# Kernel optimization log

Measured on AMD Instinct MI355X. Metric: run time of the kernel, lower is better.

Reference implementation:

```python
import jax, jax.numpy as jnp
import numpy as np

# ---- PGA G(3,0,1) tables (metric: e0^2=0, e1^2=e2^2=e3^2=1) ----
METRIC = np.array([0.0, 1.0, 1.0, 1.0])
BLADES = [(), (0,), (1,), (2,), (3,), (0, 1), (0, 2), (0, 3), (1, 2), (1, 3),
          (2, 3), (0, 1, 2), (0, 1, 3), (0, 2, 3), (1, 2, 3), (0, 1, 2, 3)]
IDX = {b: i for i, b in enumerate(BLADES)}


def _sort_sign(lst):
    lst = list(lst)
    sign = 1
    for i in range(len(lst)):
        for j in range(len(lst) - 1 - i):
            if lst[j] > lst[j + 1]:
                lst[j], lst[j + 1] = lst[j + 1], lst[j]
                sign = -sign
    return lst, sign


def _gp(a, b):
    lst, sign = _sort_sign(list(a) + list(b))
    coef = float(sign)
    out, i = [], 0
    while i < len(lst):
        if i + 1 < len(lst) and lst[i] == lst[i + 1]:
            coef *= METRIC[lst[i]]
            i += 2
        else:
            out.append(lst[i])
            i += 1
    return tuple(out), coef


def _outer(a, b):
    if set(a) & set(b):
        return (), 0.0
    lst, sign = _sort_sign(list(a) + list(b))
    return tuple(lst), float(sign)


def _build_tables():
    G = np.zeros((16, 16, 16))
    O = np.zeros((16, 16, 16))
    for i, a in enumerate(BLADES):
        for j, b in enumerate(BLADES):
            bl, c = _gp(a, b)
            if c != 0.0:
                G[IDX[bl], i, j] = c
            bl, c = _outer(a, b)
            if c != 0.0:
                O[IDX[bl], i, j] = c
    # right complement dual: a ^ dual(a) = e0123
    D = np.zeros((16, 16))
    for i, a in enumerate(BLADES):
        comp = tuple(sorted(set(range(4)) - set(a)))
        _, s = _outer(a, comp)
        D[IDX[comp], i] = s
    Dinv = np.linalg.inv(D)
    # join(x, y) = undual(dual(x) ^ dual(y))
    J = np.einsum('km,mpq,pi,qj->kij', Dinv, O, D, D)
    # 9 Pin(3,0,1)-equivariant linear basis maps:
    # 5 grade projections + 4 maps (e0 wedge grade-k part without e0)
    B = np.zeros((9, 16, 16))
    grades = [len(b) for b in BLADES]
    for w in range(5):
        for i, g in enumerate(grades):
            if g == w:
                B[w, i, i] = 1.0
    for w in range(4):
        for i, a in enumerate(BLADES):
            if len(a) == w and 0 not in a:
                bl, c = _outer((0,), a)
                B[5 + w, IDX[bl], i] = c
    return jnp.asarray(G), jnp.asarray(J), jnp.asarray(B)


GP_TBL, JOIN_TBL, EQUI_BASIS = _build_tables()


def equi_linear(x, W):
    # x: [..., c, 16], W: [o, c, 9] -> [..., o, 16]
    M = jnp.einsum('ocw,wab->oacb', W, EQUI_BASIS)  # small: [o,16,c,16]
    return jnp.einsum('oacb,...cb->...oa', M, x)


def setup_inputs() -> dict:
    key = jax.random.key(0)
    k1, k2, k3, k4 = jax.random.split(key, 4)
    B, S, C = 8, 8192, 32
    x = jax.random.normal(k1, (B, S, C, 16), dtype=jnp.float32)
    ref_mv = jax.random.normal(k2, (B, S, 1, 16), dtype=jnp.float32)
    W_bil = jax.random.normal(k3, (2 * 32, C, 9), dtype=jnp.float32) / np.sqrt(9 * C)
    W_out = jax.random.normal(k4, (C, 32, 9), dtype=jnp.float32) / np.sqrt(9 * 32)
    return {"x": x, "ref_mv": ref_mv, "W_bil": W_bil, "W_out": W_out}


def reference(x, ref_mv, W_bil, W_out):
    # project hidden channels -> 2*intermediate = 64 channels
    h = equi_linear(x, W_bil)                      # [B,S,64,16]
    lg, rg, lj, rj = jnp.split(h, 4, axis=-2)      # each [B,S,16,16]
    gp = jnp.einsum('kij,...ci,...cj->...ck', GP_TBL, lg, rg)
    jn = ref_mv[..., 14:15] * jnp.einsum('kij,...ci,...cj->...ck', JOIN_TBL, lj, rj)
    y = jnp.concatenate([gp, jn], axis=-2)         # [B,S,32,16]
    return equi_linear(y, W_out)                   # [B,S,32,16]
```

## Files before the change

kernel.cpp:

```cpp
#include <hip/hip_runtime.h>

typedef float v2f __attribute__((ext_vector_type(2)));

namespace pga {
constexpr int MASKA[16] = {0,1,2,4,8,3,5,9,6,10,12,7,11,13,14,15};
constexpr int IMASK[16] = {0,1,2,5,3,6,8,11,4,7,9,12,10,13,14,15};
constexpr int GR[16]    = {0,1,1,1,1,2,2,2,2,2,2,3,3,3,3,4};

constexpr int osign(int a, int b){
  int c = 0;
  for (int j = 0; j < 4; ++j) if ((b>>j)&1)
    for (int i = j+1; i < 4; ++i) if ((a>>i)&1) ++c;
  return (c&1) ? -1 : 1;
}

struct Tab {
  float gpc[16][16]; int gpk[16][16];
  float jnc[16][16]; int jnk[16][16];
};

constexpr Tab build(){
  Tab t{};
  for (int i = 0; i < 16; ++i) for (int j = 0; j < 16; ++j) {
    const int ma = MASKA[i], mb = MASKA[j];
    if (ma & mb & 1) { t.gpc[i][j] = 0.0f; t.gpk[i][j] = 0; }
    else { t.gpk[i][j] = IMASK[ma^mb]; t.gpc[i][j] = (float)osign(ma, mb); }
    const int ua = 15^ma, ub = 15^mb;
    if (ua & ub) { t.jnc[i][j] = 0.0f; t.jnk[i][j] = 0; }
    else {
      const int sa = osign(ma, ua), sb = osign(mb, ub);
      const int m  = ua | ub;
      const int tt = osign(ua, ub);
      const int r  = 15^m;
      const int sr = osign(r, m);
      t.jnk[i][j] = IMASK[r];
      t.jnc[i][j] = (float)(sa*sb*tt*sr);
    }
  }
  return t;
}
constexpr Tab TAB = build();
constexpr int PS[8] = {0,2,3,4,8,9,10,14};
constexpr int PE[8] = {1,5,6,7,11,12,13,15};
}

__device__ __forceinline__ float sel4(float a, float b, float c, float d, int k){
  float lo = (k & 1) ? b : a;
  float hi = (k & 1) ? d : c;
  return (k & 2) ? hi : lo;
}
__device__ __forceinline__ float xadd1(float v){
  return v + __int_as_float(__builtin_amdgcn_update_dpp(0, __float_as_int(v), 0xB1, 0xF, 0xF, false));
}
__device__ __forceinline__ float xadd2(float v){
  return v + __int_as_float(__builtin_amdgcn_update_dpp(0, __float_as_int(v), 0x4E, 0xF, 0xF, false));
}

#define NP 8
#define XS_PITCH 576
#define HS_BASE  4608
#define HS_PPITCH 1284
#define HS_OPITCH 20

template <int Q0>
__device__ __forceinline__ void equi2_half(const float* __restrict__ yb,
                                           const v2f (&WC)[4][9], v2f (&acc)[8]) {
  #pragma unroll
  for (int q = Q0; q < Q0 + 4; ++q) {
    const int s = pga::PS[q], e = pga::PE[q];
    const int js = s - (Q0/4)*8, je = e - (Q0/4)*8;
    float4 s0 = *(const float4*)(yb + s*36);
    float4 s1 = *(const float4*)(yb + s*36 + 4);
    float4 t0 = *(const float4*)(yb + e*36);
    float4 t1 = *(const float4*)(yb + e*36 + 4);
    v2f ys2[4] = { {s0.x,s0.y},{s0.z,s0.w},{s1.x,s1.y},{s1.z,s1.w} };
    v2f ye2[4] = { {t0.x,t0.y},{t0.z,t0.w},{t1.x,t1.y},{t1.z,t1.w} };
    const int gs = pga::GR[s], ge = pga::GR[e];
    #pragma unroll
    for (int cp = 0; cp < 4; ++cp) {
      acc[js] += WC[cp][gs]    * ys2[cp];
      acc[je] += WC[cp][ge]    * ye2[cp];
      acc[je] += WC[cp][4+ge]  * ys2[cp];
    }
  }
}

__launch_bounds__(256, 2)
__global__ void pga_fused(const float* __restrict__ x, const float* __restrict__ refmv,
                          const float* __restrict__ Wb, const float* __restrict__ Wo,
                          float* __restrict__ out)
{
  __shared__ float lds[14880];
  const int tid = threadIdx.x;
  const long long pos0 = (long long)blockIdx.x * NP;

  const int oA = tid >> 2, cbA = tid & 3;
  v2f WA[4][9];
  {
    const float* wb = Wb + (size_t)(oA*32 + cbA*8)*9;
    #pragma unroll
    for (int cp = 0; cp < 4; ++cp)
      #pragma unroll
      for (int w = 0; w < 9; ++w)
        WA[cp][w] = (v2f){ wb[(2*cp)*9 + w], wb[(2*cp+1)*9 + w] };
  }

  {
    const float4* xg = (const float4*)(x + pos0*512);
    #pragma unroll
    for (int r = 0; r < 4; ++r) {
      int idx = tid + 256*r;
      float4 g = xg[idx];
      int p = idx >> 7, c = (idx >> 2) & 31, aq = idx & 3;
      float* b = &lds[p*XS_PITCH + c];
      b[(aq*4+0)*36] = g.x;
      b[(aq*4+1)*36] = g.y;
      b[(aq*4+2)*36] = g.z;
      b[(aq*4+3)*36] = g.w;
    }
  }
  __syncthreads();

  #pragma unroll 1
  for (int p = 0; p < NP; ++p) {
    const float* xb = &lds[p*XS_PITCH + cbA*8];
    v2f acc[16];
    #pragma unroll
    for (int a = 0; a < 16; ++a) acc[a] = (v2f){0.f, 0.f};
    #pragma unroll
    for (int q = 0; q < 8; ++q) {
      const int s = pga::PS[q], e = pga::PE[q];
      float4 s0 = *(const float4*)(xb + s*36);
      float4 s1 = *(const float4*)(xb + s*36 + 4);
      float4 t0 = *(const float4*)(xb + e*36);
      float4 t1 = *(const float4*)(xb + e*36 + 4);
      v2f xs2[4] = { {s0.x,s0.y},{s0.z,s0.w},{s1.x,s1.y},{s1.z,s1.w} };
      v2f xe2[4] = { {t0.x,t0.y},{t0.z,t0.w},{t1.x,t1.y},{t1.z,t1.w} };
      const int gs = pga::GR[s], ge = pga::GR[e];
      #pragma unroll
      for (int cp = 0; cp < 4; ++cp) {
        acc[s] += WA[cp][gs]   * xs2[cp];
        acc[e] += WA[cp][ge]   * xe2[cp];
        acc[e] += WA[cp][4+ge] * xs2[cp];
      }
    }
    float h[16];
    #pragma unroll
    for (int a = 0; a < 16; ++a) h[a] = xadd2(xadd1(acc[a].x + acc[a].y));
    float4 v;
    v.x = sel4(h[0], h[4], h[8],  h[12], cbA);
    v.y = sel4(h[1], h[5], h[9],  h[13], cbA);
    v.z = sel4(h[2], h[6], h[10], h[14], cbA);
    v.w = sel4(h[3], h[7], h[11], h[15], cbA);
    *(float4*)&lds[HS_BASE + p*HS_PPITCH + oA*HS_OPITCH + cbA*4] = v;
  }
  __syncthreads();

  {
    const int half = tid >> 7, pb = (tid >> 4) & 7, cc = tid & 15;
    const float* r0 = &lds[HS_BASE + pb*HS_PPITCH + (half*32 + cc)*HS_OPITCH];
    const float* r1 = r0 + 16*HS_OPITCH;
    float L[16], R[16];
    #pragma unroll
    for (int k = 0; k < 4; ++k) {
      *(float4*)&L[k*4] = *(const float4*)(r0 + k*4);
      *(float4*)&R[k*4] = *(const float4*)(r1 + k*4);
    }
    float acc[16];
    #pragma unroll
    for (int k = 0; k < 16; ++k) acc[k] = 0.f;
    if (half == 0) {
      #pragma unroll
      for (int i = 0; i < 16; ++i)
        #pragma unroll
        for (int j = 0; j < 16; ++j)
          if (pga::TAB.gpc[i][j] != 0.0f)
            acc[pga::TAB.gpk[i][j]] = fmaf(pga::TAB.gpc[i][j]*L[i], R[j], acc[pga::TAB.gpk[i][j]]);
    } else {
      #pragma unroll
      for (int i = 0; i < 16; ++i)
        #pragma unroll
        for (int j = 0; j < 16; ++j)
          if (pga::TAB.jnc[i][j] != 0.0f)
            acc[pga::TAB.jnk[i][j]] = fmaf(pga::TAB.jnc[i][j]*L[i], R[j], acc[pga::TAB.jnk[i][j]]);
      const float s = refmv[(pos0 + pb)*16 + 14];
      #pragma unroll
      for (int k = 0; k < 16; ++k) acc[k] *= s;
    }
    float* yb = &lds[pb*XS_PITCH + (half*16 + cc)];
    #pragma unroll
    for (int a = 0; a < 16; ++a) yb[a*36] = acc[a];
  }

  const int ahC = tid >> 7, oC = (tid >> 2) & 31, cbC = tid & 3;
  v2f WC[4][9];
  {
    const float* wo = Wo + (size_t)(oC*32 + cbC*8)*9;
    #pragma unroll
    for (int cp = 0; cp < 4; ++cp)
      #pragma unroll
      for (int w = 0; w < 9; ++w)
        WC[cp][w] = (v2f){ wo[(2*cp)*9 + w], wo[(2*cp+1)*9 + w] };
  }
  __syncthreads();

  #pragma unroll 1
  for (int p = 0; p < NP; ++p) {
    const float* yb = &lds[p*XS_PITCH + cbC*8];
    v2f acc[8];
    #pragma unroll
    for (int j = 0; j < 8; ++j) acc[j] = (v2f){0.f, 0.f};
    if (ahC == 0) equi2_half<0>(yb, WC, acc);
    else          equi2_half<4>(yb, WC, acc);
    float f[8];
    #pragma unroll
    for (int j = 0; j < 8; ++j) f[j] = xadd2(xadd1(acc[j].x + acc[j].y));
    float2 st;
    st.x = sel4(f[0], f[2], f[4], f[6], cbC);
    st.y = sel4(f[1], f[3], f[5], f[7], cbC);
    *(float2*)&out[(pos0 + p)*512 + oC*16 + ahC*8 + cbC*2] = st;
  }
}

extern "C" void kernel_launch(void* const* d_in, const int* in_sizes, int n_in,
                              void* d_out, int out_size, void* d_ws, size_t ws_size,
                              hipStream_t stream) {
  const float* x  = (const float*)d_in[0];
  const float* rm = (const float*)d_in[1];
  const float* wb = (const float*)d_in[2];
  const float* wo = (const float*)d_in[3];
  float* out = (float*)d_out;
  const int P = in_sizes[0] / 512;
  const int blocks = P / NP;
  pga_fused<<<blocks, 256, 0, stream>>>(x, rm, wb, wo, out);
}
```

Before: 403.1 us.

## Double block threads to 512 and split per-position and bilinear work across halves

The block grows from 256 to 512 threads. In both equivariant-linear stages the thread halves take alternating positions, and in the bilinear stage the output components are split into two groups of eight handled by different threads. The aim is more parallelism and latency hiding per block with fewer serial iterations per thread. In exchange, launch_bounds(512,4) forces a tighter register budget (about 64 VGPRs per thread), which may cause spills given the 72-float weight arrays kept in registers.

```diff
diff --git a/kernel.cpp b/kernel.cpp
--- a/kernel.cpp
+++ b/kernel.cpp
@@ -85,7 +85,28 @@
   }
 }
 
-__launch_bounds__(256, 2)
+template <int KH>
+__device__ __forceinline__ void pb_gp(const float (&L)[16], const float (&R)[16], float (&acc)[8]) {
+  #pragma unroll
+  for (int i = 0; i < 16; ++i)
+    #pragma unroll
+    for (int j = 0; j < 16; ++j)
+      if (pga::TAB.gpc[i][j] != 0.0f && (pga::TAB.gpk[i][j] >> 3) == KH)
+        acc[pga::TAB.gpk[i][j] & 7] =
+          fmaf(pga::TAB.gpc[i][j]*L[i], R[j], acc[pga::TAB.gpk[i][j] & 7]);
+}
+template <int KH>
+__device__ __forceinline__ void pb_jn(const float (&L)[16], const float (&R)[16], float (&acc)[8]) {
+  #pragma unroll
+  for (int i = 0; i < 16; ++i)
+    #pragma unroll
+    for (int j = 0; j < 16; ++j)
+      if (pga::TAB.jnc[i][j] != 0.0f && (pga::TAB.jnk[i][j] >> 3) == KH)
+        acc[pga::TAB.jnk[i][j] & 7] =
+          fmaf(pga::TAB.jnc[i][j]*L[i], R[j], acc[pga::TAB.jnk[i][j] & 7]);
+}
+
+__launch_bounds__(512, 4)
 __global__ void pga_fused(const float* __restrict__ x, const float* __restrict__ refmv,
                           const float* __restrict__ Wb, const float* __restrict__ Wo,
                           float* __restrict__ out)
@@ -94,7 +115,7 @@
   const int tid = threadIdx.x;
   const long long pos0 = (long long)blockIdx.x * NP;
 
-  const int oA = tid >> 2, cbA = tid & 3;
+  const int oA = (tid >> 2) & 63, cbA = tid & 3, psA = tid >> 8;
   v2f WA[4][9];
   {
     const float* wb = Wb + (size_t)(oA*32 + cbA*8)*9;
@@ -108,8 +129,8 @@
   {
     const float4* xg = (const float4*)(x + pos0*512);
     #pragma unroll
-    for (int r = 0; r < 4; ++r) {
-      int idx = tid + 256*r;
+    for (int r = 0; r < 2; ++r) {
+      int idx = tid + 512*r;
       float4 g = xg[idx];
       int p = idx >> 7, c = (idx >> 2) & 31, aq = idx & 3;
       float* b = &lds[p*XS_PITCH + c];
@@ -122,7 +143,8 @@
   __syncthreads();
 
   #pragma unroll 1
-  for (int p = 0; p < NP; ++p) {
+  for (int it = 0; it < NP/2; ++it) {
+    const int p = 2*it + psA;
     const float* xb = &lds[p*XS_PITCH + cbA*8];
     v2f acc[16];
     #pragma unroll
@@ -157,7 +179,8 @@
   __syncthreads();
 
   {
-    const int half = tid >> 7, pb = (tid >> 4) & 7, cc = tid & 15;
+    const int cc = tid & 15, pb = (tid >> 4) & 7;
+    const int half = (tid >> 7) & 1, kh = tid >> 8;
     const float* r0 = &lds[HS_BASE + pb*HS_PPITCH + (half*32 + cc)*HS_OPITCH];
     const float* r1 = r0 + 16*HS_OPITCH;
     float L[16], R[16];
@@ -166,33 +189,23 @@
       *(float4*)&L[k*4] = *(const float4*)(r0 + k*4);
       *(float4*)&R[k*4] = *(const float4*)(r1 + k*4);
     }
-    float acc[16];
-    #pragma unroll
-    for (int k = 0; k < 16; ++k) acc[k] = 0.f;
+    float acc[8];
+    #pragma unroll
+    for (int k = 0; k < 8; ++k) acc[k] = 0.f;
     if (half == 0) {
-      #pragma unroll
-      for (int i = 0; i < 16; ++i)
-        #pragma unroll
-        for (int j = 0; j < 16; ++j)
-          if (pga::TAB.gpc[i][j] != 0.0f)
-            acc[pga::TAB.gpk[i][j]] = fmaf(pga::TAB.gpc[i][j]*L[i], R[j], acc[pga::TAB.gpk[i][j]]);
+      if (kh == 0) pb_gp<0>(L, R, acc); else pb_gp<1>(L, R, acc);
     } else {
-      #pragma unroll
-      for (int i = 0; i < 16; ++i)
-        #pragma unroll
-        for (int j = 0; j < 16; ++j)
-          if (pga::TAB.jnc[i][j] != 0.0f)
-            acc[pga::TAB.jnk[i][j]] = fmaf(pga::TAB.jnc[i][j]*L[i], R[j], acc[pga::TAB.jnk[i][j]]);
+      if (kh == 0) pb_jn<0>(L, R, acc); else pb_jn<1>(L, R, acc);
       const float s = refmv[(pos0 + pb)*16 + 14];
       #pragma unroll
-      for (int k = 0; k < 16; ++k) acc[k] *= s;
+      for (int k = 0; k < 8; ++k) acc[k] *= s;
     }
     float* yb = &lds[pb*XS_PITCH + (half*16 + cc)];
     #pragma unroll
-    for (int a = 0; a < 16; ++a) yb[a*36] = acc[a];
-  }
-
-  const int ahC = tid >> 7, oC = (tid >> 2) & 31, cbC = tid & 3;
+    for (int a = 0; a < 8; ++a) yb[(kh*8 + a)*36] = acc[a];
+  }
+
+  const int ahC = (tid >> 7) & 1, oC = (tid >> 2) & 31, cbC = tid & 3, psC = tid >> 8;
   v2f WC[4][9];
   {
     const float* wo = Wo + (size_t)(oC*32 + cbC*8)*9;
@@ -205,7 +218,8 @@
   __syncthreads();
 
   #pragma unroll 1
-  for (int p = 0; p < NP; ++p) {
+  for (int it = 0; it < NP/2; ++it) {
+    const int p = 2*it + psC;
     const float* yb = &lds[p*XS_PITCH + cbC*8];
     v2f acc[8];
     #pragma unroll
@@ -232,5 +246,5 @@
   float* out = (float*)d_out;
   const int P = in_sizes[0] / 512;
   const int blocks = P / NP;
-  pga_fused<<<blocks, 256, 0, stream>>>(x, rm, wb, wo, out);
-}
+  pga_fused<<<blocks, 512, 0, stream>>>(x, rm, wb, wo, out);
+}
```

Result: slower. 433.2 us (+7.5%).
